# Kernel tuning notes

Hardware: AMD Instinct MI355X
Metric: run time of the kernel (lower is better)

The kernel has to match this reference:

```python
import jax, jax.numpy as jnp
import numpy as np

EMBED_DIM = 256
NUM_HEADS = 8
WINDOW = 64
HEAD_DIM = EMBED_DIM // NUM_HEADS


def setup_inputs() -> dict:
    key = jax.random.key(0)
    k_x, k_w, k_ow = jax.random.split(key, 3)
    B, S, E = 2, 4096, EMBED_DIM
    x = jax.random.normal(k_x, (B, S, E), dtype=jnp.float32)
    # nn.MultiheadAttention params: packed in_proj (q,k,v) and out_proj
    bound = 1.0 / np.sqrt(E)
    in_proj_w = jax.random.uniform(k_w, (3 * E, E), jnp.float32, -bound, bound)
    in_proj_b = jnp.zeros((3 * E,), jnp.float32)
    out_w = jax.random.uniform(k_ow, (E, E), jnp.float32, -bound, bound)
    out_b = jnp.zeros((E,), jnp.float32)
    return {"x": x, "in_proj_w": in_proj_w, "in_proj_b": in_proj_b,
            "out_w": out_w, "out_b": out_b}


def reference(x, in_proj_w, in_proj_b, out_w, out_b):
    B, S, E = x.shape
    H, D = NUM_HEADS, HEAD_DIM
    # packed qkv projection (torch Linear: y = x @ W^T + b)
    qkv = jnp.einsum('bse,fe->bsf', x, in_proj_w) + in_proj_b  # [B,S,3E]
    q, k, v = jnp.split(qkv, 3, axis=-1)
    q = q.reshape(B, S, H, D).transpose(0, 2, 1, 3)  # [B,H,S,D]
    k = k.reshape(B, S, H, D).transpose(0, 2, 1, 3)
    v = v.reshape(B, S, H, D).transpose(0, 2, 1, 3)
    scale = 1.0 / jnp.sqrt(jnp.asarray(D, x.dtype))
    scores = jnp.einsum('bhqd,bhkd->bhqk', q * scale, k)  # [B,H,S,S]
    idx = jnp.arange(S)
    band = jnp.abs(idx[:, None] - idx[None, :]) <= WINDOW  # [S,S]
    neg = jnp.asarray(-1e9, scores.dtype)
    scores = jnp.where(band[None, None, :, :], scores, neg)
    attn = jax.nn.softmax(scores, axis=-1)
    out = jnp.einsum('bhqk,bhkd->bhqd', attn, v)  # [B,H,S,D]
    out = out.transpose(0, 2, 1, 3).reshape(B, S, E)
    return jnp.einsum('bse,fe->bsf', out, out_w) + out_b
```

## Files before the change

kernel.cpp:

```cpp
#include <hip/hip_runtime.h>
#include <hip/hip_bf16.h>

#define S_LEN 4096
#define EMB   256
#define NHEAD 8
#define HDIM  32
#define WIN   64
#define BATCH 2

typedef __attribute__((ext_vector_type(8))) short short8;
typedef __attribute__((ext_vector_type(4))) float floatx4;
typedef unsigned short u16;
typedef unsigned int   u32;

static __device__ __forceinline__ u32 bf16_rn(float x) {
    u32 u = __float_as_uint(x);
    return (u + 0x7FFFu + ((u >> 16) & 1u)) >> 16;
}
static __device__ __forceinline__ u32 packsplit(float x) {
    const u32 hi = bf16_rn(x);
    const float hf = __uint_as_float(hi << 16);
    const u32 lo = bf16_rn(x - hf);
    return (hi << 16) | lo;
}
static __device__ __forceinline__ void unpack_pair(u32 p0, u32 p1, u32& h, u32& l) {
    h = (p0 >> 16) | (p1 & 0xFFFF0000u);
    l = (p0 & 0xFFFFu) | (p1 << 16);
}
static __device__ __forceinline__ void unpack8(uint4 a, uint4 b, uint4& h, uint4& l) {
    unpack_pair(a.x, a.y, h.x, l.x);
    unpack_pair(a.z, a.w, h.y, l.y);
    unpack_pair(b.x, b.y, h.z, l.z);
    unpack_pair(b.z, b.w, h.w, l.w);
}

#define NX4 524288
#define NW4 49152
#define NO4 16384

__global__ __launch_bounds__(256) void convert_kernel(
    const float* __restrict__ X, const float* __restrict__ Wi, const float* __restrict__ Wo,
    u32* __restrict__ Xp, u32* __restrict__ Wip, u32* __restrict__ Wop)
{
    const int i = blockIdx.x * 256 + threadIdx.x;
    const float* src; u32* dst; int off;
    if (i < NX4)            { src = X;  dst = Xp;  off = i; }
    else if (i < NX4 + NW4) { src = Wi; dst = Wip; off = i - NX4; }
    else                    { src = Wo; dst = Wop; off = i - NX4 - NW4; }
    const float4 v = *(const float4*)(src + (size_t)off * 4);
    uint4 o;
    o.x = packsplit(v.x); o.y = packsplit(v.y);
    o.z = packsplit(v.z); o.w = packsplit(v.w);
    *(uint4*)(dst + (size_t)off * 4) = o;
}

#define LDA 40

__global__ __launch_bounds__(256) void qkv_proj_kernel(
    const u32* __restrict__ Xp, const u32* __restrict__ Wp,
    const float* __restrict__ bias,
    u32* __restrict__ Qp, u32* __restrict__ Kp, u32* __restrict__ Vp)
{
    __shared__ __align__(16) u16 Ah[128 * LDA], Al[128 * LDA];
    __shared__ __align__(16) u16 Bh[64 * LDA],  Bl[64 * LDA];
    const int tid = threadIdx.x;
    const int m0 = blockIdx.y * 128, n0 = blockIdx.x * 64;
    const int srow = tid >> 2, sc = tid & 3;
    const int lane = tid & 63, wv = tid >> 6;
    const int wm = (wv >> 1) * 64, wn = (wv & 1) * 32;
    const int lm = lane & 15, kq = lane >> 4;

    uint4 pA[2][2], pB[2];
#pragma unroll
    for (int r = 0; r < 2; ++r) {
        const u32* base = Xp + (size_t)(m0 + srow + r * 64) * EMB + sc * 8;
        pA[r][0] = *(const uint4*)base;
        pA[r][1] = *(const uint4*)(base + 4);
    }
    {
        const u32* base = Wp + (size_t)(n0 + srow) * EMB + sc * 8;
        pB[0] = *(const uint4*)base;
        pB[1] = *(const uint4*)(base + 4);
    }

    floatx4 acc[4][2] = {};
    for (int t = 0; t < 8; ++t) {
        __syncthreads();
#pragma unroll
        for (int r = 0; r < 2; ++r) {
            uint4 h, l;
            unpack8(pA[r][0], pA[r][1], h, l);
            *(uint4*)&Ah[(srow + r * 64) * LDA + sc * 8] = h;
            *(uint4*)&Al[(srow + r * 64) * LDA + sc * 8] = l;
        }
        {
            uint4 h, l;
            unpack8(pB[0], pB[1], h, l);
            *(uint4*)&Bh[srow * LDA + sc * 8] = h;
            *(uint4*)&Bl[srow * LDA + sc * 8] = l;
        }
        __syncthreads();
        if (t < 7) {
            const int k0 = (t + 1) * 32;
#pragma unroll
            for (int r = 0; r < 2; ++r) {
                const u32* base = Xp + (size_t)(m0 + srow + r * 64) * EMB + k0 + sc * 8;
                pA[r][0] = *(const uint4*)base;
                pA[r][1] = *(const uint4*)(base + 4);
            }
            const u32* base = Wp + (size_t)(n0 + srow) * EMB + k0 + sc * 8;
            pB[0] = *(const uint4*)base;
            pB[1] = *(const uint4*)(base + 4);
        }
        short8 a_h[4], a_l[4], b_h[2], b_l[2];
#pragma unroll
        for (int mt = 0; mt < 4; ++mt) {
            a_h[mt] = *(const short8*)&Ah[(wm + mt * 16 + lm) * LDA + kq * 8];
            a_l[mt] = *(const short8*)&Al[(wm + mt * 16 + lm) * LDA + kq * 8];
        }
#pragma unroll
        for (int nt = 0; nt < 2; ++nt) {
            b_h[nt] = *(const short8*)&Bh[(wn + nt * 16 + lm) * LDA + kq * 8];
            b_l[nt] = *(const short8*)&Bl[(wn + nt * 16 + lm) * LDA + kq * 8];
        }
#pragma unroll
        for (int mt = 0; mt < 4; ++mt)
#pragma unroll
            for (int nt = 0; nt < 2; ++nt) {
                acc[mt][nt] = __builtin_amdgcn_mfma_f32_16x16x32_bf16(a_h[mt], b_h[nt], acc[mt][nt], 0, 0, 0);
                acc[mt][nt] = __builtin_amdgcn_mfma_f32_16x16x32_bf16(a_h[mt], b_l[nt], acc[mt][nt], 0, 0, 0);
                acc[mt][nt] = __builtin_amdgcn_mfma_f32_16x16x32_bf16(a_l[mt], b_h[nt], acc[mt][nt], 0, 0, 0);
            }
    }
#pragma unroll
    for (int nt = 0; nt < 2; ++nt) {
        const int f = n0 + wn + nt * 16 + lm;
        const int which = f >> 8;
        const int h = (f & 255) >> 5, d = f & 31;
        u32* dst = (which == 0) ? Qp : ((which == 1) ? Kp : Vp);
        const float sc2 = (which == 0) ? 0.17677669529663687f : 1.0f;
        const float bf = bias[f];
#pragma unroll
        for (int mt = 0; mt < 4; ++mt)
#pragma unroll
            for (int r = 0; r < 4; ++r) {
                const int m = m0 + wm + mt * 16 + kq * 4 + r;
                const int b = m >> 12, s = m & (S_LEN - 1);
                dst[(((size_t)b * NHEAD + h) * S_LEN + s) * HDIM + d]
                    = packsplit((acc[mt][nt][r] + bf) * sc2);
            }
    }
}

__global__ __launch_bounds__(256) void out_proj_kernel(
    const u32* __restrict__ Abp, const u32* __restrict__ Wp,
    const float* __restrict__ bias, float* __restrict__ C)
{
    __shared__ __align__(16) u16 Ah[128 * LDA], Al[128 * LDA];
    __shared__ __align__(16) u16 Bh[64 * LDA],  Bl[64 * LDA];
    const int tid = threadIdx.x;
    const int m0 = blockIdx.y * 128, n0 = blockIdx.x * 64;
    const int srow = tid >> 2, sc = tid & 3;
    const int lane = tid & 63, wv = tid >> 6;
    const int wm = (wv >> 1) * 64, wn = (wv & 1) * 32;
    const int lm = lane & 15, kq = lane >> 4;

    uint4 pA[2][2], pB[2];
#pragma unroll
    for (int r = 0; r < 2; ++r) {
        const u32* base = Abp + (size_t)(m0 + srow + r * 64) * EMB + sc * 8;
        pA[r][0] = *(const uint4*)base;
        pA[r][1] = *(const uint4*)(base + 4);
    }
    {
        const u32* base = Wp + (size_t)(n0 + srow) * EMB + sc * 8;
        pB[0] = *(const uint4*)base;
        pB[1] = *(const uint4*)(base + 4);
    }

    floatx4 acc[4][2] = {};
    for (int t = 0; t < 8; ++t) {
        __syncthreads();
#pragma unroll
        for (int r = 0; r < 2; ++r) {
            uint4 h, l;
            unpack8(pA[r][0], pA[r][1], h, l);
            *(uint4*)&Ah[(srow + r * 64) * LDA + sc * 8] = h;
            *(uint4*)&Al[(srow + r * 64) * LDA + sc * 8] = l;
        }
        {
            uint4 h, l;
            unpack8(pB[0], pB[1], h, l);
            *(uint4*)&Bh[srow * LDA + sc * 8] = h;
            *(uint4*)&Bl[srow * LDA + sc * 8] = l;
        }
        __syncthreads();
        if (t < 7) {
            const int k0 = (t + 1) * 32;
#pragma unroll
            for (int r = 0; r < 2; ++r) {
                const u32* base = Abp + (size_t)(m0 + srow + r * 64) * EMB + k0 + sc * 8;
                pA[r][0] = *(const uint4*)base;
                pA[r][1] = *(const uint4*)(base + 4);
            }
            const u32* base = Wp + (size_t)(n0 + srow) * EMB + k0 + sc * 8;
            pB[0] = *(const uint4*)base;
            pB[1] = *(const uint4*)(base + 4);
        }
        short8 a_h[4], a_l[4], b_h[2], b_l[2];
#pragma unroll
        for (int mt = 0; mt < 4; ++mt) {
            a_h[mt] = *(const short8*)&Ah[(wm + mt * 16 + lm) * LDA + kq * 8];
            a_l[mt] = *(const short8*)&Al[(wm + mt * 16 + lm) * LDA + kq * 8];
        }
#pragma unroll
        for (int nt = 0; nt < 2; ++nt) {
            b_h[nt] = *(const short8*)&Bh[(wn + nt * 16 + lm) * LDA + kq * 8];
            b_l[nt] = *(const short8*)&Bl[(wn + nt * 16 + lm) * LDA + kq * 8];
        }
#pragma unroll
        for (int mt = 0; mt < 4; ++mt)
#pragma unroll
            for (int nt = 0; nt < 2; ++nt) {
                acc[mt][nt] = __builtin_amdgcn_mfma_f32_16x16x32_bf16(a_h[mt], b_h[nt], acc[mt][nt], 0, 0, 0);
                acc[mt][nt] = __builtin_amdgcn_mfma_f32_16x16x32_bf16(a_h[mt], b_l[nt], acc[mt][nt], 0, 0, 0);
                acc[mt][nt] = __builtin_amdgcn_mfma_f32_16x16x32_bf16(a_l[mt], b_h[nt], acc[mt][nt], 0, 0, 0);
            }
    }
#pragma unroll
    for (int nt = 0; nt < 2; ++nt) {
        const int f = n0 + wn + nt * 16 + lm;
        const float bf = bias[f];
#pragma unroll
        for (int mt = 0; mt < 4; ++mt)
#pragma unroll
            for (int r = 0; r < 4; ++r) {
                const int m = m0 + wm + mt * 16 + kq * 4 + r;
                C[(size_t)m * EMB + f] = acc[mt][nt][r] + bf;
            }
    }
}

#define AKS 40
#define AVS 224
#define APS 160

__global__ __launch_bounds__(256) void local_attn_kernel(
    const u32* __restrict__ Qp, const u32* __restrict__ Kp,
    const u32* __restrict__ Vp, u32* __restrict__ Abp)
{
    __shared__ __align__(16) u16 Qh[64 * AKS], Ql[64 * AKS];
    __shared__ __align__(16) u16 Kh[192 * AKS], Kl[192 * AKS];
    __shared__ __align__(16) u16 Vt[32 * AVS];
    __shared__ __align__(16) u16 Pw[4 * 16 * APS];

    const int tid = threadIdx.x;
    const int q0 = blockIdx.x * 64;
    const int h = blockIdx.y, b = blockIdx.z;
    const int jmin = max(0, q0 - WIN);
    const int jmax = min(S_LEN - 1, q0 + 63 + WIN);
    const int nk = jmax - jmin + 1;
    const size_t bhS = ((size_t)b * NHEAD + h) * S_LEN;
    const size_t qoff = (bhS + q0) * HDIM;
    const size_t koff = (bhS + jmin) * HDIM;

    const int srow = tid >> 2, sc = tid & 3;
    {
        const u32* base = Qp + qoff + (size_t)srow * HDIM + sc * 8;
        uint4 h4, l4;
        unpack8(*(const uint4*)base, *(const uint4*)(base + 4), h4, l4);
        *(uint4*)&Qh[srow * AKS + sc * 8] = h4;
        *(uint4*)&Ql[srow * AKS + sc * 8] = l4;
    }
#pragma unroll
    for (int r = 0; r < 3; ++r) {
        const int t = srow + r * 64;
        const int tc = min(t, nk - 1);
        const u32* base = Kp + koff + (size_t)tc * HDIM + sc * 8;
        uint4 h4, l4;
        unpack8(*(const uint4*)base, *(const uint4*)(base + 4), h4, l4);
        *(uint4*)&Kh[t * AKS + sc * 8] = h4;
        *(uint4*)&Kl[t * AKS + sc * 8] = l4;
    }
#pragma unroll
    for (int r = 0; r < 4; ++r) {
        const int t = srow + r * 64;
        if (t < 224) {
            const int tc = min(t, nk - 1);
            const u32* base = Vp + koff + (size_t)tc * HDIM + sc * 8;
            const uint4 v0 = *(const uint4*)base;
            const uint4 v1 = *(const uint4*)(base + 4);
            const int d0 = sc * 8;
            Vt[(d0 + 0) * AVS + t] = (u16)(v0.x >> 16);
            Vt[(d0 + 1) * AVS + t] = (u16)(v0.y >> 16);
            Vt[(d0 + 2) * AVS + t] = (u16)(v0.z >> 16);
            Vt[(d0 + 3) * AVS + t] = (u16)(v0.w >> 16);
            Vt[(d0 + 4) * AVS + t] = (u16)(v1.x >> 16);
            Vt[(d0 + 5) * AVS + t] = (u16)(v1.y >> 16);
            Vt[(d0 + 6) * AVS + t] = (u16)(v1.z >> 16);
            Vt[(d0 + 7) * AVS + t] = (u16)(v1.w >> 16);
        }
    }
    __syncthreads();

    const int lane = tid & 63, wv = tid >> 6;
    const int lm = lane & 15, quad = lane >> 4;
    const int qbase = wv * 16;
    const int sbase = max(0, qbase + q0 - WIN - jmin);

    const short8 qh = *(const short8*)&Qh[(qbase + lm) * AKS + quad * 8];
    const short8 ql = *(const short8*)&Ql[(qbase + lm) * AKS + quad * 8];

    floatx4 sacc[9];
#pragma unroll
    for (int nt = 0; nt < 9; ++nt) {
        const int srow2 = sbase + nt * 16 + lm;
        const short8 bh = *(const short8*)&Kh[srow2 * AKS + quad * 8];
        const short8 bl = *(const short8*)&Kl[srow2 * AKS + quad * 8];
        floatx4 a = {};
        a = __builtin_amdgcn_mfma_f32_16x16x32_bf16(qh, bh, a, 0, 0, 0);
        a = __builtin_amdgcn_mfma_f32_16x16x32_bf16(qh, bl, a, 0, 0, 0);
        a = __builtin_amdgcn_mfma_f32_16x16x32_bf16(ql, bh, a, 0, 0, 0);
        sacc[nt] = a;
    }

    const int qg = q0 + qbase + quad * 4;
    float mx[4] = {-1e30f, -1e30f, -1e30f, -1e30f};
#pragma unroll
    for (int nt = 0; nt < 9; ++nt) {
        const int slot = sbase + nt * 16 + lm;
        const int keyg = jmin + slot;
#pragma unroll
        for (int r = 0; r < 4; ++r) {
            const int qr = qg + r;
            const bool valid = (slot < nk) && (keyg >= qr - WIN) && (keyg <= qr + WIN);
            const float sv = valid ? sacc[nt][r] : -1e30f;
            sacc[nt][r] = sv;
            mx[r] = fmaxf(mx[r], sv);
        }
    }
#pragma unroll
    for (int r = 0; r < 4; ++r) {
        mx[r] = fmaxf(mx[r], __shfl_xor(mx[r], 1));
        mx[r] = fmaxf(mx[r], __shfl_xor(mx[r], 2));
        mx[r] = fmaxf(mx[r], __shfl_xor(mx[r], 4));
        mx[r] = fmaxf(mx[r], __shfl_xor(mx[r], 8));
    }
    float l[4] = {0.f, 0.f, 0.f, 0.f};
    u16* Pme = &Pw[wv * 16 * APS];
#pragma unroll
    for (int nt = 0; nt < 9; ++nt)
#pragma unroll
        for (int r = 0; r < 4; ++r) {
            const float p = __expf(sacc[nt][r] - mx[r]);
            l[r] += p;
            Pme[(quad * 4 + r) * APS + nt * 16 + lm] = (u16)bf16_rn(p);
        }
    {
        uint2 z; z.x = 0u; z.y = 0u;
        *(uint2*)&Pme[(lane >> 2) * APS + 144 + (lane & 3) * 4] = z;
    }
#pragma unroll
    for (int r = 0; r < 4; ++r) {
        l[r] += __shfl_xor(l[r], 1);
        l[r] += __shfl_xor(l[r], 2);
        l[r] += __shfl_xor(l[r], 4);
        l[r] += __shfl_xor(l[r], 8);
    }
    const float rl[4] = {1.f / l[0], 1.f / l[1], 1.f / l[2], 1.f / l[3]};

    floatx4 oacc[2] = {};
#pragma unroll
    for (int ks = 0; ks < 5; ++ks) {
        const short8 ap  = *(const short8*)&Pme[lm * APS + ks * 32 + quad * 8];
        const short8 bv0 = *(const short8*)&Vt[lm * AVS + sbase + ks * 32 + quad * 8];
        const short8 bv1 = *(const short8*)&Vt[(16 + lm) * AVS + sbase + ks * 32 + quad * 8];
        oacc[0] = __builtin_amdgcn_mfma_f32_16x16x32_bf16(ap, bv0, oacc[0], 0, 0, 0);
        oacc[1] = __builtin_amdgcn_mfma_f32_16x16x32_bf16(ap, bv1, oacc[1], 0, 0, 0);
    }
#pragma unroll
    for (int nt = 0; nt < 2; ++nt)
#pragma unroll
        for (int r = 0; r < 4; ++r) {
            const int qrow = qbase + quad * 4 + r;
            Abp[((size_t)b * S_LEN + q0 + qrow) * EMB + h * HDIM + nt * 16 + lm]
                = packsplit(oacc[nt][r] * rl[r]);
        }
}

extern "C" void kernel_launch(void* const* d_in, const int* in_sizes, int n_in,
                              void* d_out, int out_size, void* d_ws, size_t ws_size,
                              hipStream_t stream) {
    const float* x  = (const float*)d_in[0];
    const float* wi = (const float*)d_in[1];
    const float* bi = (const float*)d_in[2];
    const float* wo = (const float*)d_in[3];
    const float* bo = (const float*)d_in[4];
    float* out = (float*)d_out;

    const size_t per = (size_t)BATCH * NHEAD * S_LEN * HDIM;
    u32* p = (u32*)d_ws;
    u32* Xp  = p; p += per;
    u32* Wip = p; p += 768 * EMB;
    u32* Wop = p; p += EMB * EMB;
    u32* Qp  = p; p += per;
    u32* Kp  = p; p += per;
    u32* Vp  = p; p += per;
    u32* Abp = p; p += per;

    convert_kernel<<<dim3((NX4 + NW4 + NO4) / 256), 256, 0, stream>>>(
        x, wi, wo, Xp, Wip, Wop);
    qkv_proj_kernel<<<dim3(768 / 64, 8192 / 128), 256, 0, stream>>>(
        Xp, Wip, bi, Qp, Kp, Vp);
    local_attn_kernel<<<dim3(S_LEN / 64, NHEAD, BATCH), 256, 0, stream>>>(
        Qp, Kp, Vp, Abp);
    out_proj_kernel<<<dim3(256 / 64, 8192 / 128), 256, 0, stream>>>(
        Abp, Wop, bo, out);
}
```

Before: 112.8 us.

## Shrink out_proj tile and cut attention LDS by storing packed K/Q

```diff
diff --git a/kernel.cpp b/kernel.cpp
--- a/kernel.cpp
+++ b/kernel.cpp
@@ -32,6 +32,9 @@
     unpack_pair(a.z, a.w, h.y, l.y);
     unpack_pair(b.x, b.y, h.z, l.z);
     unpack_pair(b.z, b.w, h.w, l.w);
+}
+static __device__ __forceinline__ short8 as_short8(uint4 v) {
+    union { uint4 u; short8 s; } c; c.u = v; return c.s;
 }
 
 #define NX4 524288
@@ -156,40 +159,33 @@
     const u32* __restrict__ Abp, const u32* __restrict__ Wp,
     const float* __restrict__ bias, float* __restrict__ C)
 {
-    __shared__ __align__(16) u16 Ah[128 * LDA], Al[128 * LDA];
-    __shared__ __align__(16) u16 Bh[64 * LDA],  Bl[64 * LDA];
+    __shared__ __align__(16) u16 Ah[64 * LDA], Al[64 * LDA];
+    __shared__ __align__(16) u16 Bh[64 * LDA], Bl[64 * LDA];
     const int tid = threadIdx.x;
-    const int m0 = blockIdx.y * 128, n0 = blockIdx.x * 64;
+    const int m0 = blockIdx.y * 64, n0 = blockIdx.x * 64;
     const int srow = tid >> 2, sc = tid & 3;
     const int lane = tid & 63, wv = tid >> 6;
-    const int wm = (wv >> 1) * 64, wn = (wv & 1) * 32;
+    const int wm = (wv >> 1) * 32, wn = (wv & 1) * 32;
     const int lm = lane & 15, kq = lane >> 4;
 
-    uint4 pA[2][2], pB[2];
-#pragma unroll
-    for (int r = 0; r < 2; ++r) {
-        const u32* base = Abp + (size_t)(m0 + srow + r * 64) * EMB + sc * 8;
-        pA[r][0] = *(const uint4*)base;
-        pA[r][1] = *(const uint4*)(base + 4);
-    }
+    uint4 pA[2], pB[2];
     {
-        const u32* base = Wp + (size_t)(n0 + srow) * EMB + sc * 8;
-        pB[0] = *(const uint4*)base;
-        pB[1] = *(const uint4*)(base + 4);
-    }
-
-    floatx4 acc[4][2] = {};
+        const u32* ba = Abp + (size_t)(m0 + srow) * EMB + sc * 8;
+        pA[0] = *(const uint4*)ba;
+        pA[1] = *(const uint4*)(ba + 4);
+        const u32* bb = Wp + (size_t)(n0 + srow) * EMB + sc * 8;
+        pB[0] = *(const uint4*)bb;
+        pB[1] = *(const uint4*)(bb + 4);
+    }
+
+    floatx4 acc[2][2] = {};
     for (int t = 0; t < 8; ++t) {
         __syncthreads();
-#pragma unroll
-        for (int r = 0; r < 2; ++r) {
-            uint4 h, l;
-            unpack8(pA[r][0], pA[r][1], h, l);
-            *(uint4*)&Ah[(srow + r * 64) * LDA + sc * 8] = h;
-            *(uint4*)&Al[(srow + r * 64) * LDA + sc * 8] = l;
-        }
         {
             uint4 h, l;
+            unpack8(pA[0], pA[1], h, l);
+            *(uint4*)&Ah[srow * LDA + sc * 8] = h;
+            *(uint4*)&Al[srow * LDA + sc * 8] = l;
             unpack8(pB[0], pB[1], h, l);
             *(uint4*)&Bh[srow * LDA + sc * 8] = h;
             *(uint4*)&Bl[srow * LDA + sc * 8] = l;
@@ -197,19 +193,16 @@
         __syncthreads();
         if (t < 7) {
             const int k0 = (t + 1) * 32;
-#pragma unroll
-            for (int r = 0; r < 2; ++r) {
-                const u32* base = Abp + (size_t)(m0 + srow + r * 64) * EMB + k0 + sc * 8;
-                pA[r][0] = *(const uint4*)base;
-                pA[r][1] = *(const uint4*)(base + 4);
-            }
-            const u32* base = Wp + (size_t)(n0 + srow) * EMB + k0 + sc * 8;
-            pB[0] = *(const uint4*)base;
-            pB[1] = *(const uint4*)(base + 4);
-        }
-        short8 a_h[4], a_l[4], b_h[2], b_l[2];
-#pragma unroll
-        for (int mt = 0; mt < 4; ++mt) {
+            const u32* ba = Abp + (size_t)(m0 + srow) * EMB + k0 + sc * 8;
+            pA[0] = *(const uint4*)ba;
+            pA[1] = *(const uint4*)(ba + 4);
+            const u32* bb = Wp + (size_t)(n0 + srow) * EMB + k0 + sc * 8;
+            pB[0] = *(const uint4*)bb;
+            pB[1] = *(const uint4*)(bb + 4);
+        }
+        short8 a_h[2], a_l[2], b_h[2], b_l[2];
+#pragma unroll
+        for (int mt = 0; mt < 2; ++mt) {
             a_h[mt] = *(const short8*)&Ah[(wm + mt * 16 + lm) * LDA + kq * 8];
             a_l[mt] = *(const short8*)&Al[(wm + mt * 16 + lm) * LDA + kq * 8];
         }
@@ -219,7 +212,7 @@
             b_l[nt] = *(const short8*)&Bl[(wn + nt * 16 + lm) * LDA + kq * 8];
         }
 #pragma unroll
-        for (int mt = 0; mt < 4; ++mt)
+        for (int mt = 0; mt < 2; ++mt)
 #pragma unroll
             for (int nt = 0; nt < 2; ++nt) {
                 acc[mt][nt] = __builtin_amdgcn_mfma_f32_16x16x32_bf16(a_h[mt], b_h[nt], acc[mt][nt], 0, 0, 0);
@@ -232,7 +225,7 @@
         const int f = n0 + wn + nt * 16 + lm;
         const float bf = bias[f];
 #pragma unroll
-        for (int mt = 0; mt < 4; ++mt)
+        for (int mt = 0; mt < 2; ++mt)
 #pragma unroll
             for (int r = 0; r < 4; ++r) {
                 const int m = m0 + wm + mt * 16 + kq * 4 + r;
@@ -241,18 +234,17 @@
     }
 }
 
-#define AKS 40
-#define AVS 224
+#define KPS 36
+#define AVS 216
 #define APS 160
 
 __global__ __launch_bounds__(256) void local_attn_kernel(
     const u32* __restrict__ Qp, const u32* __restrict__ Kp,
     const u32* __restrict__ Vp, u32* __restrict__ Abp)
 {
-    __shared__ __align__(16) u16 Qh[64 * AKS], Ql[64 * AKS];
-    __shared__ __align__(16) u16 Kh[192 * AKS], Kl[192 * AKS];
+    __shared__ __align__(16) u32 Qs[64 * KPS];
+    __shared__ __align__(16) u32 Ks[192 * KPS];
     __shared__ __align__(16) u16 Vt[32 * AVS];
-    __shared__ __align__(16) u16 Pw[4 * 16 * APS];
 
     const int tid = threadIdx.x;
     const int q0 = blockIdx.x * 64;
@@ -266,26 +258,22 @@
 
     const int srow = tid >> 2, sc = tid & 3;
     {
-        const u32* base = Qp + qoff + (size_t)srow * HDIM + sc * 8;
-        uint4 h4, l4;
-        unpack8(*(const uint4*)base, *(const uint4*)(base + 4), h4, l4);
-        *(uint4*)&Qh[srow * AKS + sc * 8] = h4;
-        *(uint4*)&Ql[srow * AKS + sc * 8] = l4;
+        const u32* src = Qp + qoff + (size_t)srow * HDIM + sc * 8;
+        *(uint4*)&Qs[srow * KPS + sc * 8]     = *(const uint4*)src;
+        *(uint4*)&Qs[srow * KPS + sc * 8 + 4] = *(const uint4*)(src + 4);
     }
 #pragma unroll
     for (int r = 0; r < 3; ++r) {
         const int t = srow + r * 64;
         const int tc = min(t, nk - 1);
-        const u32* base = Kp + koff + (size_t)tc * HDIM + sc * 8;
-        uint4 h4, l4;
-        unpack8(*(const uint4*)base, *(const uint4*)(base + 4), h4, l4);
-        *(uint4*)&Kh[t * AKS + sc * 8] = h4;
-        *(uint4*)&Kl[t * AKS + sc * 8] = l4;
+        const u32* src = Kp + koff + (size_t)tc * HDIM + sc * 8;
+        *(uint4*)&Ks[t * KPS + sc * 8]     = *(const uint4*)src;
+        *(uint4*)&Ks[t * KPS + sc * 8 + 4] = *(const uint4*)(src + 4);
     }
 #pragma unroll
     for (int r = 0; r < 4; ++r) {
         const int t = srow + r * 64;
-        if (t < 224) {
+        if (t < 216) {
             const int tc = min(t, nk - 1);
             const u32* base = Vp + koff + (size_t)tc * HDIM + sc * 8;
             const uint4 v0 = *(const uint4*)base;
@@ -308,15 +296,25 @@
     const int qbase = wv * 16;
     const int sbase = max(0, qbase + q0 - WIN - jmin);
 
-    const short8 qh = *(const short8*)&Qh[(qbase + lm) * AKS + quad * 8];
-    const short8 ql = *(const short8*)&Ql[(qbase + lm) * AKS + quad * 8];
+    short8 qh, ql;
+    {
+        const uint4 p0 = *(const uint4*)&Qs[(qbase + lm) * KPS + quad * 8];
+        const uint4 p1 = *(const uint4*)&Qs[(qbase + lm) * KPS + quad * 8 + 4];
+        uint4 h4, l4;
+        unpack8(p0, p1, h4, l4);
+        qh = as_short8(h4); ql = as_short8(l4);
+    }
 
     floatx4 sacc[9];
 #pragma unroll
     for (int nt = 0; nt < 9; ++nt) {
-        const int srow2 = sbase + nt * 16 + lm;
-        const short8 bh = *(const short8*)&Kh[srow2 * AKS + quad * 8];
-        const short8 bl = *(const short8*)&Kl[srow2 * AKS + quad * 8];
+        const int row = sbase + nt * 16 + lm;
+        const uint4 p0 = *(const uint4*)&Ks[row * KPS + quad * 8];
+        const uint4 p1 = *(const uint4*)&Ks[row * KPS + quad * 8 + 4];
+        uint4 h4, l4;
+        unpack8(p0, p1, h4, l4);
+        const short8 bh = as_short8(h4);
+        const short8 bl = as_short8(l4);
         floatx4 a = {};
         a = __builtin_amdgcn_mfma_f32_16x16x32_bf16(qh, bh, a, 0, 0, 0);
         a = __builtin_amdgcn_mfma_f32_16x16x32_bf16(qh, bl, a, 0, 0, 0);
@@ -346,8 +344,12 @@
         mx[r] = fmaxf(mx[r], __shfl_xor(mx[r], 4));
         mx[r] = fmaxf(mx[r], __shfl_xor(mx[r], 8));
     }
+
+    __syncthreads();
+    u16* Pw = (u16*)Ks;
+    u16* Pme = &Pw[wv * 16 * APS];
+
     float l[4] = {0.f, 0.f, 0.f, 0.f};
-    u16* Pme = &Pw[wv * 16 * APS];
 #pragma unroll
     for (int nt = 0; nt < 9; ++nt)
 #pragma unroll
@@ -414,6 +416,6 @@
         Xp, Wip, bi, Qp, Kp, Vp);
     local_attn_kernel<<<dim3(S_LEN / 64, NHEAD, BATCH), 256, 0, stream>>>(
         Qp, Kp, Vp, Abp);
-    out_proj_kernel<<<dim3(256 / 64, 8192 / 128), 256, 0, stream>>>(
+    out_proj_kernel<<<dim3(256 / 64, 8192 / 64), 256, 0, stream>>>(
         Abp, Wop, bo, out);
 }
```

Result: no change. 114.9 us (+1.8%).
